# Kernel tuning notes

Measured on AMD Instinct MI355X. Metric: run time of the kernel, lower is better.

The kernel has to match this reference:

```python
import jax, jax.numpy as jnp
import numpy as np

BATCH, DIM, HEADS = 512, 2048, 16
CPH = DIM // HEADS  # per-head channels = 128
EPS = 1e-5


def setup_inputs() -> dict:
    key = jax.random.key(0)
    ks = jax.random.split(key, 6)
    x = jax.random.normal(ks[0], (BATCH, DIM, 1, 1), dtype=jnp.float32)
    W_qv = jax.random.normal(ks[1], (2 * DIM, DIM), dtype=jnp.float32) * (1.0 / np.sqrt(DIM))
    temperature = jnp.ones((HEADS, 1, 1), dtype=jnp.float32)
    k_param = jax.random.normal(ks[2], (BATCH, DIM, 1, 1), dtype=jnp.float32)
    bias_param = jax.random.normal(ks[3], (BATCH, HEADS, CPH * CPH, 1), dtype=jnp.float32)
    bn_gamma = jnp.ones((HEADS,), dtype=jnp.float32)
    bn_beta = jnp.zeros((HEADS,), dtype=jnp.float32)
    W_out = jax.random.normal(ks[4], (DIM, DIM, 1, 1), dtype=jnp.float32) * (1.0 / np.sqrt(DIM))
    b_out = jax.random.normal(ks[5], (DIM,), dtype=jnp.float32) * 0.01
    return {"x": x, "W_qv": W_qv, "temperature": temperature, "k_param": k_param,
            "bias_param": bias_param, "bn_gamma": bn_gamma, "bn_beta": bn_beta,
            "W_out": W_out, "b_out": b_out}


def reference(x, W_qv, temperature, k_param, bias_param, bn_gamma, bn_beta, W_out, b_out):
    b, c, h, w = x.shape  # h = w = 1 (required by x.squeeze() + Linear)
    heads = temperature.shape[0]
    cph = c // heads

    xs = x.reshape(b, c)
    qv = xs @ W_qv.T                     # [b, 2c]
    q, v = qv[:, :c], qv[:, c:]
    q = q.reshape(b, heads, cph, 1)      # b head c (h w)
    v = v.reshape(b, heads, cph, 1)
    k = k_param.reshape(b, heads, cph, 1)

    # BatchNorm2d over channel = head (training-mode batch stats, biased var)
    mean = jnp.mean(v, axis=(0, 2, 3), keepdims=True)
    var = jnp.var(v, axis=(0, 2, 3), keepdims=True)
    v = (v - mean) * jax.lax.rsqrt(var + EPS)
    v = v * bn_gamma.reshape(1, heads, 1, 1) + bn_beta.reshape(1, heads, 1, 1)

    # attn = q @ k^T over the singleton spatial dim -> [b, head, cph, cph]
    attn = jnp.einsum('bhcx,bhdx->bhcd', q, k)
    attn = attn + bias_param.reshape(b, heads, cph, cph)
    attn = attn * temperature  # [heads,1,1] broadcasts over batch
    attn = jax.nn.softmax(attn, axis=-1)

    out = jnp.einsum('bhcd,bhdx->bhcx', attn, v)  # [b, head, cph, 1]
    out = out.reshape(b, c)

    # 1x1 conv == matmul
    out = out @ W_out.reshape(c, c).T + b_out
    return out.reshape(b, c, 1, 1)
```

## Files before the change

kernel.cpp:

```cpp
#include <hip/hip_runtime.h>
#include <hip/hip_bf16.h>
#include <cstdint>

#define NBATCH 512
#define NDIM   2048
#define NHEADS 16
#define NCPH   128

typedef __bf16 bf16x8 __attribute__((ext_vector_type(8)));
typedef float  f32x4  __attribute__((ext_vector_type(4)));

__device__ __forceinline__ unsigned short f2bf(float f) {
    uint32_t u = __builtin_bit_cast(uint32_t, f);
    u += 0x7FFFu + ((u >> 16) & 1u);
    return (unsigned short)(u >> 16);
}

template<int BM, int BN, int BK, bool A_BF16, bool BNP>
__global__ __launch_bounds__(256) void gemm_deep(
    const unsigned short* __restrict__ Abf, const float* __restrict__ Af,
    const float* __restrict__ Bf, float* __restrict__ C,
    const float* __restrict__ bias, float* __restrict__ bnpart,
    int M, int N, int K)
{
    constexpr int WM = BM / 2, WN = BN / 2;
    constexpr int MI = WM / 16, NI = WN / 16;
    constexpr int CPR = BK / 8;
    constexpr int RNA = (BM * BK) / 2048;
    constexpr int RNB = (BN * BK) / 2048;

    __shared__ unsigned short As[2][BM * BK];
    __shared__ unsigned short Bs[2][BN * BK];

    const int tid  = threadIdx.x;
    const int lane = tid & 63;
    const int wid  = tid >> 6;
    const int wr   = wid >> 1;
    const int wc   = wid & 1;
    const int m0   = blockIdx.y * BM;
    const int n0   = blockIdx.x * BN;
    const int fr   = lane & 15;
    const int kq   = lane >> 4;

    f32x4 acc[MI][NI] = {};

    float4 fA0[A_BF16 ? 1 : RNA][2], fA1[A_BF16 ? 1 : RNA][2];
    bf16x8 hA0[A_BF16 ? RNA : 1],    hA1[A_BF16 ? RNA : 1];
    float4 fB0[RNB][2], fB1[RNB][2];

    auto loadA = [&](auto& fa, auto& ha, int k0) {
        if constexpr (A_BF16) {
#pragma unroll
            for (int r = 0; r < RNA; r++) {
                const int e = r * 2048 + tid * 8;
                const int row = e / BK, cb = e % BK;
                ha[r] = *(const bf16x8*)(Abf + (size_t)(m0 + row) * K + k0 + cb);
            }
        } else {
#pragma unroll
            for (int r = 0; r < RNA; r++) {
                const int idx = r * 256 + tid;
                const int row = idx / CPR, cc = idx % CPR;
                const float4* g = (const float4*)(Af + (size_t)(m0 + row) * K
                                                  + k0 + cc * 8);
                fa[r][0] = g[0];
                fa[r][1] = g[1];
            }
        }
    };
    auto loadB = [&](auto& fb, int k0) {
#pragma unroll
        for (int r = 0; r < RNB; r++) {
            const int idx = r * 256 + tid;
            const int row = idx / CPR, cc = idx % CPR;
            const float4* g = (const float4*)(Bf + (size_t)(n0 + row) * K
                                              + k0 + cc * 8);
            fb[r][0] = g[0];
            fb[r][1] = g[1];
        }
    };
    auto writeA = [&](int bs, auto& fa, auto& ha) {
        if constexpr (A_BF16) {
#pragma unroll
            for (int r = 0; r < RNA; r++) {
                const int e = r * 2048 + tid * 8;
                const int row = e / BK, cc = (e % BK) >> 3;
                *(bf16x8*)&As[bs][row * BK + ((cc ^ (row & 7)) << 3)] = ha[r];
            }
        } else {
#pragma unroll
            for (int r = 0; r < RNA; r++) {
                const int idx = r * 256 + tid;
                const int row = idx / CPR, cc = idx % CPR;
                bf16x8 v;
                v[0] = (__bf16)fa[r][0].x; v[1] = (__bf16)fa[r][0].y;
                v[2] = (__bf16)fa[r][0].z; v[3] = (__bf16)fa[r][0].w;
                v[4] = (__bf16)fa[r][1].x; v[5] = (__bf16)fa[r][1].y;
                v[6] = (__bf16)fa[r][1].z; v[7] = (__bf16)fa[r][1].w;
                *(bf16x8*)&As[bs][row * BK + ((cc ^ (row & 7)) << 3)] = v;
            }
        }
    };
    auto writeB = [&](int bs, auto& fb) {
#pragma unroll
        for (int r = 0; r < RNB; r++) {
            const int idx = r * 256 + tid;
            const int row = idx / CPR, cc = idx % CPR;
            bf16x8 v;
            v[0] = (__bf16)fb[r][0].x; v[1] = (__bf16)fb[r][0].y;
            v[2] = (__bf16)fb[r][0].z; v[3] = (__bf16)fb[r][0].w;
            v[4] = (__bf16)fb[r][1].x; v[5] = (__bf16)fb[r][1].y;
            v[6] = (__bf16)fb[r][1].z; v[7] = (__bf16)fb[r][1].w;
            *(bf16x8*)&Bs[bs][row * BK + ((cc ^ (row & 7)) << 3)] = v;
        }
    };
    auto compute = [&](int bs) {
#pragma unroll
        for (int kh = 0; kh < BK / 32; kh++) {
            const int kchunk = kh * 4 + kq;
            bf16x8 af[MI], bfv[NI];
#pragma unroll
            for (int i = 0; i < MI; i++) {
                const int row = wr * WM + i * 16 + fr;
                af[i] = *(const bf16x8*)&As[bs][row * BK
                        + ((kchunk ^ (row & 7)) << 3)];
            }
#pragma unroll
            for (int j = 0; j < NI; j++) {
                const int row = wc * WN + j * 16 + fr;
                bfv[j] = *(const bf16x8*)&Bs[bs][row * BK
                         + ((kchunk ^ (row & 7)) << 3)];
            }
#pragma unroll
            for (int i = 0; i < MI; i++)
#pragma unroll
                for (int j = 0; j < NI; j++)
                    acc[i][j] = __builtin_amdgcn_mfma_f32_16x16x32_bf16(
                        af[i], bfv[j], acc[i][j], 0, 0, 0);
        }
    };
    auto barrier = [&]() {
        asm volatile("s_waitcnt lgkmcnt(0)" ::: "memory");
        __builtin_amdgcn_s_barrier();
        __builtin_amdgcn_sched_barrier(0);
    };

    loadA(fA0, hA0, 0);
    loadB(fB0, 0);
    loadA(fA1, hA1, BK);
    loadB(fB1, BK);
    writeA(0, fA0, hA0);
    writeB(0, fB0);
    barrier();

    const int NT = K / BK;
    for (int t = 0; t < NT; t += 2) {
        if (t + 2 < NT) { loadA(fA0, hA0, (t + 2) * BK); loadB(fB0, (t + 2) * BK); }
        compute(0);
        writeA(1, fA1, hA1);
        writeB(1, fB1);
        barrier();
        if (t + 3 < NT) { loadA(fA1, hA1, (t + 3) * BK); loadB(fB1, (t + 3) * BK); }
        compute(1);
        if (t + 2 < NT) {
            writeA(0, fA0, hA0);
            writeB(0, fB0);
            barrier();
        }
    }

    const int row0 = m0 + wr * WM + (kq << 2);
    const int col0 = n0 + wc * WN + fr;
#pragma unroll
    for (int j = 0; j < NI; j++) {
        const int cc = col0 + j * 16;
        const float badd = bias ? bias[cc] : 0.0f;
#pragma unroll
        for (int i = 0; i < MI; i++)
#pragma unroll
            for (int r = 0; r < 4; r++)
                C[(size_t)(row0 + i * 16 + r) * N + cc] = acc[i][j][r] + badd;
    }

    if (BNP && n0 >= NDIM) {
        float s = 0.f, ss = 0.f;
#pragma unroll
        for (int i = 0; i < MI; i++)
#pragma unroll
            for (int j = 0; j < NI; j++)
#pragma unroll
                for (int r = 0; r < 4; r++) {
                    const float v = acc[i][j][r];
                    s += v;
                    ss = fmaf(v, v, ss);
                }
#pragma unroll
        for (int off = 32; off; off >>= 1) {
            s  += __shfl_down(s, off);
            ss += __shfl_down(ss, off);
        }
        __shared__ float rs[4], rss[4];
        if (lane == 0) { rs[wid] = s; rss[wid] = ss; }
        __syncthreads();
        if (tid == 0)
            ((float2*)bnpart)[((n0 - NDIM) >> 6) * 8 + (m0 >> 6)] =
                make_float2(rs[0] + rs[1] + rs[2] + rs[3],
                            rss[0] + rss[1] + rss[2] + rss[3]);
    }
}

__global__ __launch_bounds__(256) void attn_k(
    const float* __restrict__ qv, const float* __restrict__ kparam,
    const float* __restrict__ bias, const float* __restrict__ temperature,
    const float* __restrict__ bnpart, const float* __restrict__ gamma,
    const float* __restrict__ beta, unsigned short* __restrict__ aout)
{
    const int bh2 = blockIdx.x;
    const int bh  = bh2 >> 1, rh = bh2 & 1;
    const int b   = bh >> 4,  h  = bh & 15;
    const int tid = threadIdx.x;

    __shared__ float ks[NCPH], vsr[NCPH], s2sh[2];
    if (tid < 32)
        ((float4*)ks)[tid] =
            ((const float4*)(kparam + (size_t)b * NDIM + h * NCPH))[tid];
    else if (tid < 64)
        ((float4*)vsr)[tid - 32] =
            ((const float4*)(qv + (size_t)b * (2 * NDIM) + NDIM + h * NCPH))[tid - 32];

    if (tid < 16) {
        float2 p = ((const float2*)bnpart)[(h * 2 + (tid >> 3)) * 8 + (tid & 7)];
        float s = p.x, ss = p.y;
#pragma unroll
        for (int off = 8; off; off >>= 1) {
            s  += __shfl_xor(s, off);
            ss += __shfl_xor(ss, off);
        }
        if (tid == 0) {
            const float inv = 1.0f / (NBATCH * NCPH);
            float mean = s * inv;
            float var  = ss * inv - mean * mean;
            float scl  = gamma[h] * rsqrtf(var + 1e-5f);
            s2sh[0] = scl;
            s2sh[1] = beta[h] - mean * scl;
        }
    }

    const int c  = rh * 64 + (tid >> 2);
    const int q4 = tid & 3;
    const float qc   = qv[(size_t)b * (2 * NDIM) + h * NCPH + c];
    const float temp = temperature[h];

    const float4* bp = (const float4*)(bias + ((size_t)bh << 14)
                                       + (size_t)c * NCPH + q4 * 32);
    float4 l4[8];
#pragma unroll
    for (int j = 0; j < 8; j++) l4[j] = bp[j];

    __syncthreads();
    const float scl = s2sh[0], shf = s2sh[1];
    const float4* kk4 = (const float4*)(ks  + q4 * 32);
    const float4* vv4 = (const float4*)(vsr + q4 * 32);

    float s0 = 0.f, s1 = 0.f, o0 = 0.f, o1 = 0.f;
#pragma unroll
    for (int j = 0; j < 8; j++) {
        const float4 bb = l4[j];
        const float4 kx = kk4[j];
        const float4 vx = vv4[j];
        float px = __expf(fmaf(qc, kx.x, bb.x) * temp);
        float py = __expf(fmaf(qc, kx.y, bb.y) * temp);
        float pz = __expf(fmaf(qc, kx.z, bb.z) * temp);
        float pw = __expf(fmaf(qc, kx.w, bb.w) * temp);
        s0 += px; s1 += py; s0 += pz; s1 += pw;
        o0 = fmaf(px, vx.x, o0);
        o1 = fmaf(py, vx.y, o1);
        o0 = fmaf(pz, vx.z, o0);
        o1 = fmaf(pw, vx.w, o1);
    }
    float s = s0 + s1, o = o0 + o1;
    s += __shfl_xor(s, 1);
    o += __shfl_xor(o, 1);
    s += __shfl_xor(s, 2);
    o += __shfl_xor(o, 2);

    if (q4 == 0)
        aout[(size_t)b * NDIM + h * NCPH + c] = f2bf(fmaf(scl, o / s, shf));
}

extern "C" void kernel_launch(void* const* d_in, const int* in_sizes, int n_in,
                              void* d_out, int out_size, void* d_ws, size_t ws_size,
                              hipStream_t stream)
{
    const float* x      = (const float*)d_in[0];
    const float* Wqv    = (const float*)d_in[1];
    const float* temp   = (const float*)d_in[2];
    const float* kparam = (const float*)d_in[3];
    const float* bias   = (const float*)d_in[4];
    const float* gamma  = (const float*)d_in[5];
    const float* beta   = (const float*)d_in[6];
    const float* Wout   = (const float*)d_in[7];
    const float* bout   = (const float*)d_in[8];
    float* out = (float*)d_out;

    char* ws = (char*)d_ws;
    float*          qv     = (float*)(ws);
    unsigned short* ao_bf  = (unsigned short*)(ws + 8388608);
    float*          bnpart = (float*)(ws + 10485760);

    gemm_deep<64, 64, 64, false, true><<<dim3(64, 8), 256, 0, stream>>>(
        nullptr, x, Wqv, qv, nullptr, bnpart, NBATCH, 2 * NDIM, NDIM);

    attn_k<<<2 * NBATCH * NHEADS, 256, 0, stream>>>(
        qv, kparam, bias, temp, bnpart, gamma, beta, ao_bf);

    gemm_deep<64, 32, 64, true, false><<<dim3(64, 8), 256, 0, stream>>>(
        ao_bf, nullptr, Wout, out, bout, nullptr, NBATCH, NDIM, NDIM);
}
```

Before: 165.8 us.

## Split-K both GEMMs with separate reduction and BatchNorm-stat kernels

Both GEMMs now use split-K (2-way for the QV projection, 4-way for the output projection) with BK reduced to 32. Each K-slice writes fp32 partials that new reduce kernels sum, adding bias for the output. BatchNorm statistics move from the GEMM epilogue into the first reduce plus a one-block finalize kernel, and attention reads precomputed scale and shift. The aim is more blocks in flight on a machine with many compute units, at the cost of extra partial-buffer traffic and three additional kernel launches.

```diff
diff --git a/kernel.cpp b/kernel.cpp
--- a/kernel.cpp
+++ b/kernel.cpp
@@ -16,18 +16,15 @@
     return (unsigned short)(u >> 16);
 }
 
-template<int BM, int BN, int BK, bool A_BF16, bool BNP>
-__global__ __launch_bounds__(256) void gemm_deep(
+template<int BM, int BN, int BK, bool A_BF16>
+__global__ __launch_bounds__(256, 4) void gemm_sk(
     const unsigned short* __restrict__ Abf, const float* __restrict__ Af,
-    const float* __restrict__ Bf, float* __restrict__ C,
-    const float* __restrict__ bias, float* __restrict__ bnpart,
-    int M, int N, int K)
+    const float* __restrict__ Bf, float* __restrict__ Cpart,
+    int M, int N, int K, int KS)
 {
     constexpr int WM = BM / 2, WN = BN / 2;
     constexpr int MI = WM / 16, NI = WN / 16;
     constexpr int CPR = BK / 8;
-    constexpr int RNA = (BM * BK) / 2048;
-    constexpr int RNB = (BN * BK) / 2048;
 
     __shared__ unsigned short As[2][BM * BK];
     __shared__ unsigned short Bs[2][BN * BK];
@@ -39,105 +36,72 @@
     const int wc   = wid & 1;
     const int m0   = blockIdx.y * BM;
     const int n0   = blockIdx.x * BN;
+    const int kbase = blockIdx.z * KS;
     const int fr   = lane & 15;
     const int kq   = lane >> 4;
 
     f32x4 acc[MI][NI] = {};
 
-    float4 fA0[A_BF16 ? 1 : RNA][2], fA1[A_BF16 ? 1 : RNA][2];
-    bf16x8 hA0[A_BF16 ? RNA : 1],    hA1[A_BF16 ? RNA : 1];
-    float4 fB0[RNB][2], fB1[RNB][2];
-
-    auto loadA = [&](auto& fa, auto& ha, int k0) {
+    float4 fA0[2], fA1[2], fB0[2], fB1[2];
+    bf16x8 hA0, hA1;
+
+    const int arow = tid / CPR, acc8 = tid % CPR;
+    const int brow = tid / CPR, bcc8 = tid % CPR;
+
+    auto loadA = [&](float4* fa, bf16x8& ha, int k0) {
         if constexpr (A_BF16) {
-#pragma unroll
-            for (int r = 0; r < RNA; r++) {
-                const int e = r * 2048 + tid * 8;
-                const int row = e / BK, cb = e % BK;
-                ha[r] = *(const bf16x8*)(Abf + (size_t)(m0 + row) * K + k0 + cb);
-            }
+            ha = *(const bf16x8*)(Abf + (size_t)(m0 + arow) * K + k0 + acc8 * 8);
         } else {
-#pragma unroll
-            for (int r = 0; r < RNA; r++) {
-                const int idx = r * 256 + tid;
-                const int row = idx / CPR, cc = idx % CPR;
-                const float4* g = (const float4*)(Af + (size_t)(m0 + row) * K
-                                                  + k0 + cc * 8);
-                fa[r][0] = g[0];
-                fa[r][1] = g[1];
-            }
-        }
-    };
-    auto loadB = [&](auto& fb, int k0) {
-#pragma unroll
-        for (int r = 0; r < RNB; r++) {
-            const int idx = r * 256 + tid;
-            const int row = idx / CPR, cc = idx % CPR;
-            const float4* g = (const float4*)(Bf + (size_t)(n0 + row) * K
-                                              + k0 + cc * 8);
-            fb[r][0] = g[0];
-            fb[r][1] = g[1];
-        }
-    };
-    auto writeA = [&](int bs, auto& fa, auto& ha) {
+            const float4* g = (const float4*)(Af + (size_t)(m0 + arow) * K
+                                              + k0 + acc8 * 8);
+            fa[0] = g[0];
+            fa[1] = g[1];
+        }
+    };
+    auto loadB = [&](float4* fb, int k0) {
+        const float4* g = (const float4*)(Bf + (size_t)(n0 + brow) * K
+                                          + k0 + bcc8 * 8);
+        fb[0] = g[0];
+        fb[1] = g[1];
+    };
+    auto writeA = [&](int bs, float4* fa, bf16x8& ha) {
         if constexpr (A_BF16) {
-#pragma unroll
-            for (int r = 0; r < RNA; r++) {
-                const int e = r * 2048 + tid * 8;
-                const int row = e / BK, cc = (e % BK) >> 3;
-                *(bf16x8*)&As[bs][row * BK + ((cc ^ (row & 7)) << 3)] = ha[r];
-            }
+            *(bf16x8*)&As[bs][arow * BK + ((acc8 ^ (arow & 3)) << 3)] = ha;
         } else {
-#pragma unroll
-            for (int r = 0; r < RNA; r++) {
-                const int idx = r * 256 + tid;
-                const int row = idx / CPR, cc = idx % CPR;
-                bf16x8 v;
-                v[0] = (__bf16)fa[r][0].x; v[1] = (__bf16)fa[r][0].y;
-                v[2] = (__bf16)fa[r][0].z; v[3] = (__bf16)fa[r][0].w;
-                v[4] = (__bf16)fa[r][1].x; v[5] = (__bf16)fa[r][1].y;
-                v[6] = (__bf16)fa[r][1].z; v[7] = (__bf16)fa[r][1].w;
-                *(bf16x8*)&As[bs][row * BK + ((cc ^ (row & 7)) << 3)] = v;
-            }
-        }
-    };
-    auto writeB = [&](int bs, auto& fb) {
-#pragma unroll
-        for (int r = 0; r < RNB; r++) {
-            const int idx = r * 256 + tid;
-            const int row = idx / CPR, cc = idx % CPR;
             bf16x8 v;
-            v[0] = (__bf16)fb[r][0].x; v[1] = (__bf16)fb[r][0].y;
-            v[2] = (__bf16)fb[r][0].z; v[3] = (__bf16)fb[r][0].w;
-            v[4] = (__bf16)fb[r][1].x; v[5] = (__bf16)fb[r][1].y;
-            v[6] = (__bf16)fb[r][1].z; v[7] = (__bf16)fb[r][1].w;
-            *(bf16x8*)&Bs[bs][row * BK + ((cc ^ (row & 7)) << 3)] = v;
-        }
+            v[0] = (__bf16)fa[0].x; v[1] = (__bf16)fa[0].y;
+            v[2] = (__bf16)fa[0].z; v[3] = (__bf16)fa[0].w;
+            v[4] = (__bf16)fa[1].x; v[5] = (__bf16)fa[1].y;
+            v[6] = (__bf16)fa[1].z; v[7] = (__bf16)fa[1].w;
+            *(bf16x8*)&As[bs][arow * BK + ((acc8 ^ (arow & 3)) << 3)] = v;
+        }
+    };
+    auto writeB = [&](int bs, float4* fb) {
+        bf16x8 v;
+        v[0] = (__bf16)fb[0].x; v[1] = (__bf16)fb[0].y;
+        v[2] = (__bf16)fb[0].z; v[3] = (__bf16)fb[0].w;
+        v[4] = (__bf16)fb[1].x; v[5] = (__bf16)fb[1].y;
+        v[6] = (__bf16)fb[1].z; v[7] = (__bf16)fb[1].w;
+        *(bf16x8*)&Bs[bs][brow * BK + ((bcc8 ^ (brow & 3)) << 3)] = v;
     };
     auto compute = [&](int bs) {
-#pragma unroll
-        for (int kh = 0; kh < BK / 32; kh++) {
-            const int kchunk = kh * 4 + kq;
-            bf16x8 af[MI], bfv[NI];
-#pragma unroll
-            for (int i = 0; i < MI; i++) {
-                const int row = wr * WM + i * 16 + fr;
-                af[i] = *(const bf16x8*)&As[bs][row * BK
-                        + ((kchunk ^ (row & 7)) << 3)];
-            }
-#pragma unroll
-            for (int j = 0; j < NI; j++) {
-                const int row = wc * WN + j * 16 + fr;
-                bfv[j] = *(const bf16x8*)&Bs[bs][row * BK
-                         + ((kchunk ^ (row & 7)) << 3)];
-            }
-#pragma unroll
-            for (int i = 0; i < MI; i++)
-#pragma unroll
-                for (int j = 0; j < NI; j++)
-                    acc[i][j] = __builtin_amdgcn_mfma_f32_16x16x32_bf16(
-                        af[i], bfv[j], acc[i][j], 0, 0, 0);
-        }
+        bf16x8 af[MI], bfv[NI];
+#pragma unroll
+        for (int i = 0; i < MI; i++) {
+            const int row = wr * WM + i * 16 + fr;
+            af[i] = *(const bf16x8*)&As[bs][row * BK + ((kq ^ (row & 3)) << 3)];
+        }
+#pragma unroll
+        for (int j = 0; j < NI; j++) {
+            const int row = wc * WN + j * 16 + fr;
+            bfv[j] = *(const bf16x8*)&Bs[bs][row * BK + ((kq ^ (row & 3)) << 3)];
+        }
+#pragma unroll
+        for (int i = 0; i < MI; i++)
+#pragma unroll
+            for (int j = 0; j < NI; j++)
+                acc[i][j] = __builtin_amdgcn_mfma_f32_16x16x32_bf16(
+                    af[i], bfv[j], acc[i][j], 0, 0, 0);
     };
     auto barrier = [&]() {
         asm volatile("s_waitcnt lgkmcnt(0)" ::: "memory");
@@ -145,22 +109,24 @@
         __builtin_amdgcn_sched_barrier(0);
     };
 
-    loadA(fA0, hA0, 0);
-    loadB(fB0, 0);
-    loadA(fA1, hA1, BK);
-    loadB(fB1, BK);
+    loadA(fA0, hA0, kbase);
+    loadB(fB0, kbase);
+    loadA(fA1, hA1, kbase + BK);
+    loadB(fB1, kbase + BK);
     writeA(0, fA0, hA0);
     writeB(0, fB0);
     barrier();
 
-    const int NT = K / BK;
+    const int NT = KS / BK;
     for (int t = 0; t < NT; t += 2) {
-        if (t + 2 < NT) { loadA(fA0, hA0, (t + 2) * BK); loadB(fB0, (t + 2) * BK); }
+        if (t + 2 < NT) { loadA(fA0, hA0, kbase + (t + 2) * BK);
+                          loadB(fB0, kbase + (t + 2) * BK); }
         compute(0);
         writeA(1, fA1, hA1);
         writeB(1, fB1);
         barrier();
-        if (t + 3 < NT) { loadA(fA1, hA1, (t + 3) * BK); loadB(fB1, (t + 3) * BK); }
+        if (t + 3 < NT) { loadA(fA1, hA1, kbase + (t + 3) * BK);
+                          loadB(fB1, kbase + (t + 3) * BK); }
         compute(1);
         if (t + 2 < NT) {
             writeA(0, fA0, hA0);
@@ -169,58 +135,91 @@
         }
     }
 
+    float* Cp = Cpart + (size_t)blockIdx.z * M * N;
     const int row0 = m0 + wr * WM + (kq << 2);
     const int col0 = n0 + wc * WN + fr;
 #pragma unroll
     for (int j = 0; j < NI; j++) {
         const int cc = col0 + j * 16;
-        const float badd = bias ? bias[cc] : 0.0f;
 #pragma unroll
         for (int i = 0; i < MI; i++)
 #pragma unroll
             for (int r = 0; r < 4; r++)
-                C[(size_t)(row0 + i * 16 + r) * N + cc] = acc[i][j][r] + badd;
-    }
-
-    if (BNP && n0 >= NDIM) {
+                Cp[(size_t)(row0 + i * 16 + r) * N + cc] = acc[i][j][r];
+    }
+}
+
+__global__ __launch_bounds__(256) void reduce1(
+    const float* __restrict__ part, float* __restrict__ qv,
+    float* __restrict__ bnpart)
+{
+    const int b = blockIdx.x, t = threadIdx.x;
+    const size_t row = (size_t)b * (2 * NDIM);
+    const size_t sks = (size_t)NBATCH * (2 * NDIM);
+    float4 acc[4];
+#pragma unroll
+    for (int f = 0; f < 4; f++) {
+        const size_t off = row + t * 16 + f * 4;
+        float4 a = *(const float4*)&part[off];
+        float4 c = *(const float4*)&part[sks + off];
+        acc[f] = make_float4(a.x + c.x, a.y + c.y, a.z + c.z, a.w + c.w);
+        *(float4*)&qv[off] = acc[f];
+    }
+    if (t >= 128) {
         float s = 0.f, ss = 0.f;
 #pragma unroll
-        for (int i = 0; i < MI; i++)
-#pragma unroll
-            for (int j = 0; j < NI; j++)
-#pragma unroll
-                for (int r = 0; r < 4; r++) {
-                    const float v = acc[i][j][r];
-                    s += v;
-                    ss = fmaf(v, v, ss);
-                }
-#pragma unroll
-        for (int off = 32; off; off >>= 1) {
-            s  += __shfl_down(s, off);
-            ss += __shfl_down(ss, off);
-        }
-        __shared__ float rs[4], rss[4];
-        if (lane == 0) { rs[wid] = s; rss[wid] = ss; }
-        __syncthreads();
-        if (tid == 0)
-            ((float2*)bnpart)[((n0 - NDIM) >> 6) * 8 + (m0 >> 6)] =
-                make_float2(rs[0] + rs[1] + rs[2] + rs[3],
-                            rss[0] + rss[1] + rss[2] + rss[3]);
+        for (int f = 0; f < 4; f++) {
+            s  += acc[f].x + acc[f].y + acc[f].z + acc[f].w;
+            ss = fmaf(acc[f].x, acc[f].x, fmaf(acc[f].y, acc[f].y,
+                 fmaf(acc[f].z, acc[f].z, fmaf(acc[f].w, acc[f].w, ss))));
+        }
+#pragma unroll
+        for (int off = 1; off < 8; off <<= 1) {
+            s  += __shfl_xor(s, off);
+            ss += __shfl_xor(ss, off);
+        }
+        if ((t & 7) == 0)
+            ((float2*)bnpart)[b * NHEADS + ((t - 128) >> 3)] = make_float2(s, ss);
+    }
+}
+
+__global__ __launch_bounds__(256) void bn_final(
+    const float* __restrict__ bnpart, const float* __restrict__ gamma,
+    const float* __restrict__ beta, float* __restrict__ sc2)
+{
+    const int t = threadIdx.x;
+    const int h = t >> 4, j = t & 15;
+    float s = 0.f, ss = 0.f;
+#pragma unroll
+    for (int i = 0; i < 32; i++) {
+        float2 p = ((const float2*)bnpart)[(j + 16 * i) * NHEADS + h];
+        s += p.x; ss += p.y;
+    }
+#pragma unroll
+    for (int off = 1; off < 16; off <<= 1) {
+        s  += __shfl_xor(s, off);
+        ss += __shfl_xor(ss, off);
+    }
+    if (j == 0) {
+        const float inv = 1.0f / (NBATCH * NCPH);
+        float mean = s * inv;
+        float var  = ss * inv - mean * mean;
+        float scl  = gamma[h] * rsqrtf(var + 1e-5f);
+        ((float2*)sc2)[h] = make_float2(scl, beta[h] - mean * scl);
     }
 }
 
 __global__ __launch_bounds__(256) void attn_k(
     const float* __restrict__ qv, const float* __restrict__ kparam,
     const float* __restrict__ bias, const float* __restrict__ temperature,
-    const float* __restrict__ bnpart, const float* __restrict__ gamma,
-    const float* __restrict__ beta, unsigned short* __restrict__ aout)
+    const float* __restrict__ sc2, unsigned short* __restrict__ aout)
 {
     const int bh2 = blockIdx.x;
     const int bh  = bh2 >> 1, rh = bh2 & 1;
     const int b   = bh >> 4,  h  = bh & 15;
     const int tid = threadIdx.x;
 
-    __shared__ float ks[NCPH], vsr[NCPH], s2sh[2];
+    __shared__ float ks[NCPH], vsr[NCPH];
     if (tid < 32)
         ((float4*)ks)[tid] =
             ((const float4*)(kparam + (size_t)b * NDIM + h * NCPH))[tid];
@@ -228,28 +227,11 @@
         ((float4*)vsr)[tid - 32] =
             ((const float4*)(qv + (size_t)b * (2 * NDIM) + NDIM + h * NCPH))[tid - 32];
 
-    if (tid < 16) {
-        float2 p = ((const float2*)bnpart)[(h * 2 + (tid >> 3)) * 8 + (tid & 7)];
-        float s = p.x, ss = p.y;
-#pragma unroll
-        for (int off = 8; off; off >>= 1) {
-            s  += __shfl_xor(s, off);
-            ss += __shfl_xor(ss, off);
-        }
-        if (tid == 0) {
-            const float inv = 1.0f / (NBATCH * NCPH);
-            float mean = s * inv;
-            float var  = ss * inv - mean * mean;
-            float scl  = gamma[h] * rsqrtf(var + 1e-5f);
-            s2sh[0] = scl;
-            s2sh[1] = beta[h] - mean * scl;
-        }
-    }
-
     const int c  = rh * 64 + (tid >> 2);
     const int q4 = tid & 3;
     const float qc   = qv[(size_t)b * (2 * NDIM) + h * NCPH + c];
     const float temp = temperature[h];
+    const float2 s2  = ((const float2*)sc2)[h];
 
     const float4* bp = (const float4*)(bias + ((size_t)bh << 14)
                                        + (size_t)c * NCPH + q4 * 32);
@@ -258,7 +240,6 @@
     for (int j = 0; j < 8; j++) l4[j] = bp[j];
 
     __syncthreads();
-    const float scl = s2sh[0], shf = s2sh[1];
     const float4* kk4 = (const float4*)(ks  + q4 * 32);
     const float4* vv4 = (const float4*)(vsr + q4 * 32);
 
@@ -285,7 +266,32 @@
     o += __shfl_xor(o, 2);
 
     if (q4 == 0)
-        aout[(size_t)b * NDIM + h * NCPH + c] = f2bf(fmaf(scl, o / s, shf));
+        aout[(size_t)b * NDIM + h * NCPH + c] = f2bf(fmaf(s2.x, o / s, s2.y));
+}
+
+__global__ __launch_bounds__(256) void reduce2(
+    const float* __restrict__ part, float* __restrict__ outp,
+    const float* __restrict__ bout)
+{
+    const int b = blockIdx.x, t = threadIdx.x;
+    const size_t row = (size_t)b * NDIM;
+    const size_t sks = (size_t)NBATCH * NDIM;
+#pragma unroll
+    for (int f = 0; f < 2; f++) {
+        const size_t off = row + t * 8 + f * 4;
+        const int col = t * 8 + f * 4;
+        float4 a = *(const float4*)&part[off];
+        float4 c = *(const float4*)&part[sks + off];
+        float4 d = *(const float4*)&part[2 * sks + off];
+        float4 e = *(const float4*)&part[3 * sks + off];
+        float4 bb = *(const float4*)&bout[col];
+        float4 r;
+        r.x = a.x + c.x + d.x + e.x + bb.x;
+        r.y = a.y + c.y + d.y + e.y + bb.y;
+        r.z = a.z + c.z + d.z + e.z + bb.z;
+        r.w = a.w + c.w + d.w + e.w + bb.w;
+        *(float4*)&outp[off] = r;
+    }
 }
 
 extern "C" void kernel_launch(void* const* d_in, const int* in_sizes, int n_in,
@@ -306,14 +312,23 @@
     char* ws = (char*)d_ws;
     float*          qv     = (float*)(ws);
     unsigned short* ao_bf  = (unsigned short*)(ws + 8388608);
-    float*          bnpart = (float*)(ws + 10485760);
-
-    gemm_deep<64, 64, 64, false, true><<<dim3(64, 8), 256, 0, stream>>>(
-        nullptr, x, Wqv, qv, nullptr, bnpart, NBATCH, 2 * NDIM, NDIM);
+    float*          part1  = (float*)(ws + 10485760);
+    float*          part2  = (float*)(ws + 27262976);
+    float*          bnpart = (float*)(ws + 44040192);
+    float*          sc2    = (float*)(ws + 44105728);
+
+    gemm_sk<64, 64, 32, false><<<dim3(64, 8, 2), 256, 0, stream>>>(
+        nullptr, x, Wqv, part1, NBATCH, 2 * NDIM, NDIM, NDIM / 2);
+
+    reduce1<<<NBATCH, 256, 0, stream>>>(part1, qv, bnpart);
+
+    bn_final<<<1, 256, 0, stream>>>(bnpart, gamma, beta, sc2);
 
     attn_k<<<2 * NBATCH * NHEADS, 256, 0, stream>>>(
-        qv, kparam, bias, temp, bnpart, gamma, beta, ao_bf);
-
-    gemm_deep<64, 32, 64, true, false><<<dim3(64, 8), 256, 0, stream>>>(
-        ao_bf, nullptr, Wout, out, bout, nullptr, NBATCH, NDIM, NDIM);
-}
+        qv, kparam, bias, temp, sc2, ao_bf);
+
+    gemm_sk<64, 64, 32, true><<<dim3(32, 8, 4), 256, 0, stream>>>(
+        ao_bf, nullptr, Wout, part2, NBATCH, NDIM, NDIM, NDIM / 4);
+
+    reduce2<<<NBATCH, 256, 0, stream>>>(part2, out, bout);
+}
```

After: 188.4 us. 1.14x slower.
